# Performance work log

Hardware: AMD Instinct MI355X
Metric: run time of the kernel (lower is better)

Reference implementation:

```python
import jax, jax.numpy as jnp
import numpy as np

N, P, H, K = 8192, 32, 512, 100
D = 2 * P
R = 32  # min(32, max(8, H))


def setup_inputs() -> dict:
    key = jax.random.key(0)
    ks = jax.random.split(key, 12)
    # strictly increasing event times
    dts = jax.random.uniform(ks[0], (N,), dtype=jnp.float32) * 0.1 + 1e-3
    times = jnp.cumsum(dts)
    marks = jax.random.randint(ks[1], (N,), 0, K, dtype=jnp.int32)
    u_inputs = jax.random.normal(ks[2], (N, H), dtype=jnp.float32) * 0.1
    # parameters (match torch init scales)
    lambda_log_real = jax.random.normal(ks[3], (P,), dtype=jnp.float32) * 0.1
    lambda_im = jax.random.normal(ks[4], (P,), dtype=jnp.float32) * 0.05
    V = jnp.eye(D, dtype=jnp.float32) + 0.01 * jax.random.normal(ks[5], (D, D), dtype=jnp.float32)
    B = jax.random.normal(ks[6], (D, H), dtype=jnp.float32) * 0.05
    E = jax.random.normal(ks[7], (D, R), dtype=jnp.float32) * 0.05
    alpha = jax.random.normal(ks[8], (R, K), dtype=jnp.float32) * 0.05
    gate_w = jax.random.normal(ks[9], (P, H), dtype=jnp.float32) * 0.02
    gate_b = jax.random.normal(ks[10], (P,), dtype=jnp.float32) * 0.02
    x0 = jnp.zeros((D,), dtype=jnp.float32)
    return {"times": times, "marks": marks, "u_inputs": u_inputs,
            "lambda_log_real": lambda_log_real, "lambda_im": lambda_im,
            "V": V, "B": B, "E": E, "alpha": alpha,
            "gate_w": gate_w, "gate_b": gate_b, "x0": x0}


def _v_block(V, pr, pi):
    """V @ blockdiag_p([[pr,-pi],[pi,pr]]) for each step n. V:(D,D), pr/pi:(n,P) -> (n,D,D)."""
    Dd = V.shape[0]
    Pp = pr.shape[-1]
    Vr = V.reshape(Dd, Pp, 2)
    col0 = Vr[None, :, :, 0] * pr[:, None, :] + Vr[None, :, :, 1] * pi[:, None, :]
    col1 = -Vr[None, :, :, 0] * pi[:, None, :] + Vr[None, :, :, 1] * pr[:, None, :]
    return jnp.stack([col0, col1], axis=-1).reshape(-1, Dd, Dd)


def reference(times, marks, u_inputs, lambda_log_real, lambda_im, V, B, E, alpha, gate_w, gate_b, x0):
    n = times.shape[0]
    dt = jnp.concatenate([times[:1], jnp.diff(times)])  # (N,) t_0 - 0, t_i - t_{i-1}
    # input-dependent eigenvalues: real = -softplus(log_real) * softplus(Wu+b), imag fixed
    gate = jax.nn.softplus(u_inputs @ gate_w.T + gate_b)           # (N,P)
    real = -jax.nn.softplus(lambda_log_real)[None, :] * gate        # (N,P)
    imag = jnp.broadcast_to(lambda_im[None, :], real.shape)         # (N,P)
    dtc = dt[:, None]
    exps = jnp.exp(real * dtc)
    cosb = jnp.cos(imag * dtc)
    sinb = jnp.sin(imag * dtc)
    a = exps * cosb  # Re(exp(lam dt))
    c = exps * sinb  # Im(exp(lam dt))
    V_inv = jnp.linalg.inv(V)
    # exp(A dt) = V M V^{-1}, M block-rotation per mode
    Aexp = _v_block(V, a, c) @ V_inv                                # (N,D,D)
    # integral (exp(lam dt) - 1)/lam, with dt fallback near lam=0
    denom = real * real + imag * imag
    num_re = a - 1.0
    num_im = c
    qr = (num_re * real + num_im * imag) / (denom + 1e-12)
    qi = (num_im * real - num_re * imag) / (denom + 1e-12)
    small = denom < 1e-8
    qr = jnp.where(small, dtc, qr)
    qi = jnp.where(small, 0.0, qi)
    VMint = _v_block(V, qr, qi)                                     # (N,D,D)
    # cont = V M_int V^{-1} B u  (fuse V^{-1} B u first, avoiding Kmat materialization)
    w = u_inputs @ (V_inv @ B).T                                    # (N,D)
    cont = jnp.einsum('nij,nj->ni', VMint, w)
    cont = jnp.where(dtc > 0, cont, 0.0)
    # mark impulses r_k = E alpha[:, k]
    r = (E @ alpha)[:, marks].T                                     # (N,D)

    def step(x_prev, inp):
        A_i, c_i, r_i = inp
        x_left = A_i @ x_prev + c_i
        x_right = x_left + r_i
        return x_right, (x_right, x_left)

    _, (x_right, x_left) = jax.lax.scan(step, x0, (Aexp, cont, r))
    return x_right, x_left
```

## Files before the change

kernel.cpp:

```cpp
#include <hip/hip_runtime.h>
#include <math.h>

#define NN 8192
#define PP 32
#define HH 512
#define KK 100
#define DD 64
#define RR 32
#define MM 96

#define CH 2
#define CPB 16
#define SB 32
#define NB 256

#define OFF_VINV   0
#define OFF_M      (OFF_VINV + DD*DD)
#define OFF_EAT    (OFF_M + DD*HH)
#define OFF_RHT    (OFF_EAT + KK*DD)
#define OFF_Y0     (OFF_RHT + KK*DD)
#define OFF_BAGG   (OFF_Y0 + DD)
#define OFF_YB     (OFF_BAGG + NB*PP*4)
#define OFF_C      (OFF_YB + NB*PP*2)
#define OFF_COEF   (OFF_C + NN*MM)

__device__ __forceinline__ float sp_fast(float x) {
    return x > 15.f ? x : __logf(1.f + __expf(x));
}
__device__ __forceinline__ float rcp_fast(float x) {
    float r;
    asm("v_rcp_f32 %0, %1" : "=v"(r) : "v"(x));
    return r;
}
__device__ __forceinline__ float4 comp_aff(float4 f, float4 g) {
    float4 r;
    r.x = f.x * g.x - f.y * g.y;
    r.y = f.x * g.y + f.y * g.x;
    r.z = f.x * g.z - f.y * g.w + f.z;
    r.w = f.x * g.w + f.y * g.z + f.w;
    return r;
}

#define IDX(r,c) ((r)*64 + ((c) ^ (((r)&7)<<2)))
__global__ __launch_bounds__(512) void kinv(const float* __restrict__ V,
                                            const float* __restrict__ x0,
                                            float* __restrict__ ws) {
    __shared__ float sm[16384];
    float* Vt = sm;
    float* X  = sm + 4096;
    float* Xt = sm + 8192;
    float* T  = sm + 12288;
    const int t  = threadIdx.x;
    const int j0 = (t & 15) << 2;
    const int i0 = (t >> 4) << 1;

    float nx[2][4];
    #pragma unroll
    for (int r = 0; r < 2; r++) {
        float4 v4 = *(const float4*)&V[(i0 + r) * DD + j0];
        float vv[4] = {v4.x, v4.y, v4.z, v4.w};
        #pragma unroll
        for (int s = 0; s < 4; s++) {
            Vt[IDX(j0 + s, i0 + r)] = vv[s];
            float xv = ((i0 + r) == (j0 + s) ? 2.f : 0.f) - vv[s];
            nx[r][s] = xv;
            Xt[IDX(j0 + s, i0 + r)] = xv;
        }
        *(float4*)&X[IDX(i0 + r, j0)] = make_float4(nx[r][0], nx[r][1], nx[r][2], nx[r][3]);
    }
    __syncthreads();

    for (int it = 0; it < 3; it++) {
        float acc[2][4];
        #pragma unroll
        for (int r = 0; r < 2; r++)
            #pragma unroll
            for (int s = 0; s < 4; s++) acc[r][s] = 0.f;
        for (int k = 0; k < DD; k++) {
            float2 a2 = *(float2*)&Vt[IDX(k, i0)];
            float4 b4 = *(float4*)&X[IDX(k, j0)];
            float bv[4] = {b4.x, b4.y, b4.z, b4.w};
            #pragma unroll
            for (int s = 0; s < 4; s++) {
                acc[0][s] = fmaf(a2.x, bv[s], acc[0][s]);
                acc[1][s] = fmaf(a2.y, bv[s], acc[1][s]);
            }
        }
        #pragma unroll
        for (int r = 0; r < 2; r++)
            *(float4*)&T[IDX(i0 + r, j0)] = make_float4(acc[r][0], acc[r][1], acc[r][2], acc[r][3]);
        __syncthreads();
        #pragma unroll
        for (int r = 0; r < 2; r++)
            #pragma unroll
            for (int s = 0; s < 4; s++) acc[r][s] = 0.f;
        for (int k = 0; k < DD; k++) {
            float2 a2 = *(float2*)&Xt[IDX(k, i0)];
            float4 b4 = *(float4*)&T[IDX(k, j0)];
            float bv[4] = {b4.x, b4.y, b4.z, b4.w};
            #pragma unroll
            for (int s = 0; s < 4; s++) {
                acc[0][s] = fmaf(a2.x, bv[s], acc[0][s]);
                acc[1][s] = fmaf(a2.y, bv[s], acc[1][s]);
            }
        }
        #pragma unroll
        for (int r = 0; r < 2; r++) {
            float4 xo = *(float4*)&X[IDX(i0 + r, j0)];
            nx[r][0] = 2.f * xo.x - acc[r][0];
            nx[r][1] = 2.f * xo.y - acc[r][1];
            nx[r][2] = 2.f * xo.z - acc[r][2];
            nx[r][3] = 2.f * xo.w - acc[r][3];
        }
        __syncthreads();
        #pragma unroll
        for (int r = 0; r < 2; r++) {
            *(float4*)&X[IDX(i0 + r, j0)] = make_float4(nx[r][0], nx[r][1], nx[r][2], nx[r][3]);
            #pragma unroll
            for (int s = 0; s < 4; s++) Xt[IDX(j0 + s, i0 + r)] = nx[r][s];
        }
        __syncthreads();
    }
    #pragma unroll
    for (int r = 0; r < 2; r++)
        *(float4*)&ws[OFF_VINV + (i0 + r) * DD + j0] =
            make_float4(nx[r][0], nx[r][1], nx[r][2], nx[r][3]);
    float4 xq = *(const float4*)&x0[j0];
    float xw[4] = {xq.x, xq.y, xq.z, xq.w};
    #pragma unroll
    for (int r = 0; r < 2; r++) {
        float pr = nx[r][0] * xw[0] + nx[r][1] * xw[1] + nx[r][2] * xw[2] + nx[r][3] * xw[3];
        T[(i0 + r) * 17 + (t & 15)] = pr;
    }
    __syncthreads();
    if (t < DD) {
        float s = 0.f;
        #pragma unroll
        for (int jt = 0; jt < 16; jt++) s += T[t * 17 + jt];
        ws[OFF_Y0 + t] = s;
    }
}

__global__ __launch_bounds__(256) void kpre(const float* __restrict__ B,
                                            const float* __restrict__ E,
                                            const float* __restrict__ alpha,
                                            float* __restrict__ ws) {
    int b = blockIdx.x, t = threadIdx.x;
    if (b < 32) {
        int d = b * 2 + (t >> 7);
        int h0 = (t & 127) * 4;
        const float* vr = ws + OFF_VINV + d * DD;
        float4 acc = {0.f, 0.f, 0.f, 0.f};
        for (int j = 0; j < DD; j++) {
            float v = vr[j];
            float4 b4 = *(const float4*)&B[j * HH + h0];
            acc.x = fmaf(v, b4.x, acc.x); acc.y = fmaf(v, b4.y, acc.y);
            acc.z = fmaf(v, b4.z, acc.z); acc.w = fmaf(v, b4.w, acc.w);
        }
        *(float4*)&ws[OFF_M + d * HH + h0] = acc;
    } else {
        __shared__ float vi[DD * 65];
        __shared__ float ea_s[4][DD];
        int kk = (b - 32) * 4 + (t >> 6);
        int d = t & 63;
        for (int idx = t; idx < DD * DD; idx += 256)
            vi[(idx >> 6) * 65 + (idx & 63)] = ws[OFF_VINV + idx];
        float ea = 0.f;
        #pragma unroll
        for (int r = 0; r < RR; r++) ea = fmaf(E[d * RR + r], alpha[r * KK + kk], ea);
        ws[OFF_EAT + kk * DD + d] = ea;
        ea_s[t >> 6][d] = ea;
        __syncthreads();
        float rr = 0.f;
        for (int j = 0; j < DD; j++) rr = fmaf(vi[d * 65 + j], ea_s[t >> 6][j], rr);
        ws[OFF_RHT + kk * DD + d] = rr;
    }
}

__global__ __launch_bounds__(256, 2) void kgemm(const float* __restrict__ u,
                                                const float* __restrict__ gate_w,
                                                float* __restrict__ ws) {
    __shared__ float uT[16 * 64];
    __shared__ float mT[96 * 64];
    int t = threadIdx.x;
    int n0 = blockIdx.x * 16;
    int tn = t & 7, tm = t >> 3;
    float acc[2][3];
    #pragma unroll
    for (int i = 0; i < 2; i++)
        #pragma unroll
        for (int j = 0; j < 3; j++) acc[i][j] = 0.f;

    for (int kc = 0; kc < HH; kc += 64) {
        {
            int r = t >> 4, c4 = t & 15;
            float4 f4 = *(const float4*)&u[(n0 + r) * HH + kc + c4 * 4];
            *(float4*)&uT[r * 64 + ((c4 ^ (r & 7)) << 2)] = f4;
        }
        #pragma unroll
        for (int s = 0; s < 6; s++) {
            int idx = t + 256 * s;
            int r = idx >> 4, c4 = idx & 15;
            const float* src = (r < 32) ? &gate_w[r * HH] : &ws[OFF_M + (r - 32) * HH];
            float4 f4 = *(const float4*)&src[kc + c4 * 4];
            *(float4*)&mT[r * 64 + ((c4 ^ (r & 7)) << 2)] = f4;
        }
        __syncthreads();
        #pragma unroll
        for (int k4 = 0; k4 < 16; k4++) {
            float4 uu[2], mm[3];
            #pragma unroll
            for (int i = 0; i < 2; i++) {
                int rr = 2 * tn + i;
                uu[i] = *(float4*)&uT[rr * 64 + ((k4 ^ (rr & 7)) << 2)];
            }
            #pragma unroll
            for (int j = 0; j < 3; j++) {
                int m = 3 * tm + j;
                mm[j] = *(float4*)&mT[m * 64 + ((k4 ^ (m & 7)) << 2)];
            }
            #pragma unroll
            for (int i = 0; i < 2; i++)
                #pragma unroll
                for (int j = 0; j < 3; j++)
                    acc[i][j] += uu[i].x * mm[j].x + uu[i].y * mm[j].y +
                                 uu[i].z * mm[j].z + uu[i].w * mm[j].w;
        }
        __syncthreads();
    }
    #pragma unroll
    for (int i = 0; i < 2; i++)
        #pragma unroll
        for (int j = 0; j < 3; j++)
            ws[OFF_C + (n0 + 2 * tn + i) * MM + 3 * tm + j] = acc[i][j];
}

__device__ __forceinline__ float4 coef_fast(const float* __restrict__ ws,
                                            const int* __restrict__ marks,
                                            int n, int p, float dtv,
                                            float nlr, float imag, float gb) {
    float gate = sp_fast(ws[OFF_C + n * MM + p] + gb);
    float real = nlr * gate;
    float e = __expf(real * dtv);
    float x = imag * dtv, x2 = x * x;
    float cb = 1.f - x2 * (0.5f - x2 * (1.f / 24.f));
    float sb = x * (1.f - x2 * ((1.f / 6.f) - x2 * (1.f / 120.f)));
    float a = e * cb, c = e * sb;
    float denom = real * real + imag * imag;
    float inv = rcp_fast(denom + 1e-12f);
    float nre = a - 1.f, nim = c;
    float qr = (nre * real + nim * imag) * inv;
    float qi = (nim * real - nre * imag) * inv;
    if (denom < 1e-8f) { qr = dtv; qi = 0.f; }
    float2 w = *(const float2*)&ws[OFF_C + n * MM + 32 + 2 * p];
    float br = qr * w.x - qi * w.y;
    float bi = qr * w.y + qi * w.x;
    if (!(dtv > 0.f)) { br = 0.f; bi = 0.f; }
    int mk = marks[n];
    float2 rh = *(const float2*)&ws[OFF_RHT + mk * DD + 2 * p];
    return make_float4(a, c, br + rh.x, bi + rh.y);
}

__global__ __launch_bounds__(512, 2) void kagg(const float* __restrict__ times,
                                               const int* __restrict__ marks,
                                               const float* __restrict__ llr,
                                               const float* __restrict__ lim,
                                               const float* __restrict__ gate_b,
                                               float* __restrict__ ws) {
    __shared__ float4 smagg[CPB][PP];
    int b = blockIdx.x, t = threadIdx.x;
    int c = t >> 5, p = t & 31;
    int n0 = b * SB + c * CH;
    float nlr = -sp_fast(llr[p]);
    float imag = lim[p], gb = gate_b[p];
    float tprev = (n0 == 0) ? 0.f : times[n0 - 1];
    float4* coef = (float4*)(ws + OFF_COEF);
    float4 agg = make_float4(1.f, 0.f, 0.f, 0.f);
    #pragma unroll
    for (int i = 0; i < CH; i++) {
        int n = n0 + i;
        float tcur = times[n];
        float dtv = tcur - tprev; tprev = tcur;
        float4 cf = coef_fast(ws, marks, n, p, dtv, nlr, imag, gb);
        coef[n * PP + p] = cf;
        agg = comp_aff(cf, agg);
    }
    smagg[c][p] = agg;
    __syncthreads();
    if (t < PP) {
        float4 T = make_float4(1.f, 0.f, 0.f, 0.f);
        #pragma unroll
        for (int cc = 0; cc < CPB; cc++) T = comp_aff(smagg[cc][t], T);
        *(float4*)&ws[OFF_BAGG + (b * PP + t) * 4] = T;
    }
}

__global__ __launch_bounds__(256) void kscan(float* __restrict__ ws) {
    __shared__ float4 sseg[8][PP];
    __shared__ float4 qseg[8][PP];
    int t = threadIdx.x;
    int p = t & 31, s = t >> 5;
    const float4* bagg = (const float4*)(ws + OFF_BAGG);
    float4 S = make_float4(1.f, 0.f, 0.f, 0.f);
    for (int b = 32 * s; b < 32 * s + 32; b++) S = comp_aff(bagg[b * PP + p], S);
    sseg[s][p] = S;
    __syncthreads();
    if (t < PP) {
        float4 Q = make_float4(1.f, 0.f, 0.f, 0.f);
        #pragma unroll
        for (int ss = 0; ss < 8; ss++) { qseg[ss][t] = Q; Q = comp_aff(sseg[ss][t], Q); }
    }
    __syncthreads();
    float2 y0v = *(const float2*)&ws[OFF_Y0 + 2 * p];
    float4 Q = qseg[s][p];
    float2 y;
    y.x = Q.x * y0v.x - Q.y * y0v.y + Q.z;
    y.y = Q.x * y0v.y + Q.y * y0v.x + Q.w;
    for (int b = 32 * s; b < 32 * s + 32; b++) {
        *(float2*)&ws[OFF_YB + (b * PP + p) * 2] = y;
        float4 A = bagg[b * PP + p];
        float nyr = A.x * y.x - A.y * y.y + A.z;
        float nyi = A.x * y.y + A.y * y.x + A.w;
        y.x = nyr; y.y = nyi;
    }
}

__global__ __launch_bounds__(512, 2) void kout(const float* __restrict__ V,
                                               const int* __restrict__ marks,
                                               const float* __restrict__ ws,
                                               float* __restrict__ out) {
    __shared__ float vt[DD * 68];
    __shared__ float yl[SB * 68];
    __shared__ float4 smagg[CPB][PP];
    int b = blockIdx.x, t = threadIdx.x;
    #pragma unroll
    for (int s = 0; s < 8; s++) {
        int idx = t + 512 * s;
        vt[(idx & 63) * 68 + (idx >> 6)] = V[idx];
    }
    int c = t >> 5, p = t & 31;
    int n0 = b * SB + c * CH;
    const float4* coef = (const float4*)(ws + OFF_COEF);
    float4 cf0 = coef[(n0 + 0) * PP + p];
    float4 cf1 = coef[(n0 + 1) * PP + p];
    smagg[c][p] = comp_aff(cf1, cf0);
    __syncthreads();
    float2 y = *(const float2*)&ws[OFF_YB + (b * PP + p) * 2];
    #pragma unroll
    for (int cc = 0; cc < CPB - 1; cc++) {
        float4 A = smagg[cc][p];
        if (cc < c) {
            float nyr = A.x * y.x - A.y * y.y + A.z;
            float nyi = A.x * y.y + A.y * y.x + A.w;
            y.x = nyr; y.y = nyi;
        }
    }
    {
        float nyr = cf0.x * y.x - cf0.y * y.y + cf0.z;
        float nyi = cf0.x * y.y + cf0.y * y.x + cf0.w;
        y.x = nyr; y.y = nyi;
        *(float2*)&yl[(c * CH + 0) * 68 + 2 * p] = y;
        nyr = cf1.x * y.x - cf1.y * y.y + cf1.z;
        nyi = cf1.x * y.y + cf1.y * y.x + cf1.w;
        y.x = nyr; y.y = nyi;
        *(float2*)&yl[(c * CH + 1) * 68 + 2 * p] = y;
    }
    __syncthreads();
    int dt4 = (t & 15) * 4;
    int nr = t >> 4;
    float acc[4] = {0.f, 0.f, 0.f, 0.f};
    for (int k = 0; k < DD; k++) {
        float4 vv = *(float4*)&vt[k * 68 + dt4];
        float yv = yl[nr * 68 + k];
        acc[0] = fmaf(yv, vv.x, acc[0]);
        acc[1] = fmaf(yv, vv.y, acc[1]);
        acc[2] = fmaf(yv, vv.z, acc[2]);
        acc[3] = fmaf(yv, vv.w, acc[3]);
    }
    int n = b * SB + nr;
    int mk = marks[n];
    float4 o4 = make_float4(acc[0], acc[1], acc[2], acc[3]);
    *(float4*)&out[n * DD + dt4] = o4;
    float4 e4 = *(const float4*)&ws[OFF_EAT + mk * DD + dt4];
    o4.x -= e4.x; o4.y -= e4.y; o4.z -= e4.z; o4.w -= e4.w;
    *(float4*)&out[NN * DD + n * DD + dt4] = o4;
}

extern "C" void kernel_launch(void* const* d_in, const int* in_sizes, int n_in,
                              void* d_out, int out_size, void* d_ws, size_t ws_size,
                              hipStream_t stream) {
    (void)in_sizes; (void)n_in; (void)out_size; (void)ws_size;
    const float* times  = (const float*)d_in[0];
    const int*   marks  = (const int*)d_in[1];
    const float* u      = (const float*)d_in[2];
    const float* llr    = (const float*)d_in[3];
    const float* lim    = (const float*)d_in[4];
    const float* V      = (const float*)d_in[5];
    const float* B      = (const float*)d_in[6];
    const float* E      = (const float*)d_in[7];
    const float* alpha  = (const float*)d_in[8];
    const float* gate_w = (const float*)d_in[9];
    const float* gate_b = (const float*)d_in[10];
    const float* x0     = (const float*)d_in[11];
    float* ws  = (float*)d_ws;
    float* out = (float*)d_out;

    hipLaunchKernelGGL(kinv,  dim3(1),   dim3(512), 0, stream, V, x0, ws);
    hipLaunchKernelGGL(kpre,  dim3(57),  dim3(256), 0, stream, B, E, alpha, ws);
    hipLaunchKernelGGL(kgemm, dim3(512), dim3(256), 0, stream, u, gate_w, ws);
    hipLaunchKernelGGL(kagg,  dim3(256), dim3(512), 0, stream, times, marks, llr, lim, gate_b, ws);
    hipLaunchKernelGGL(kscan, dim3(1),   dim3(256), 0, stream, ws);
    hipLaunchKernelGGL(kout,  dim3(256), dim3(512), 0, stream, V, marks, ws, out);
}
```

Baseline: 166.6 us.

## Fuse six kernels into one cooperative megakernel with grid syncs

Replaces the six launches (inverse, precompute, gemm, aggregate, serial scan, output) with a single cooperative kernel of 256 blocks, separated into three phases by grid-wide syncs. The gemm now multiplies by B directly, and V^{-1} is applied afterwards per block, which removes the dependency on the inverse before the gemm. The single-block serial scan becomes a per-block prefix over the block aggregates. This is meant to remove launch overhead and serial stages, but block 0 does the Newton inverse while the other blocks proceed, and each block recomputes up to 256 prefix compositions. If the cooperative launch fails, it falls back to three ordinary launches.

```diff
diff --git a/kernel.cpp b/kernel.cpp
--- a/kernel.cpp
+++ b/kernel.cpp
@@ -1,5 +1,8 @@
 #include <hip/hip_runtime.h>
+#include <hip/hip_cooperative_groups.h>
 #include <math.h>
+
+namespace cg = cooperative_groups;
 
 #define NN 8192
 #define PP 32
@@ -8,21 +11,23 @@
 #define DD 64
 #define RR 32
 #define MM 96
-
-#define CH 2
-#define CPB 16
 #define SB 32
-#define NB 256
-
-#define OFF_VINV   0
-#define OFF_M      (OFF_VINV + DD*DD)
-#define OFF_EAT    (OFF_M + DD*HH)
-#define OFF_RHT    (OFF_EAT + KK*DD)
-#define OFF_Y0     (OFF_RHT + KK*DD)
-#define OFF_BAGG   (OFF_Y0 + DD)
-#define OFF_YB     (OFF_BAGG + NB*PP*4)
-#define OFF_C      (OFF_YB + NB*PP*2)
-#define OFF_COEF   (OFF_C + NN*MM)
+#define NSEG 256
+
+#define OFF_VINV 0
+#define OFF_EAT  4096
+#define OFF_RHT  10496
+#define OFF_Y0   16896
+#define OFF_BAGG 16960
+#define OFF_C    49728
+#define OFF_COEF 836160
+
+#define L1_CT   4352
+#define L1_AG   7424
+#define L2_AG   4352
+#define L2_PREF 6400
+#define L2_YL   8448
+#define L2_YB   10624
 
 __device__ __forceinline__ float sp_fast(float x) {
     return x > 15.f ? x : __logf(1.f + __expf(x));
@@ -42,348 +47,326 @@
 }
 
 #define IDX(r,c) ((r)*64 + ((c) ^ (((r)&7)<<2)))
-__global__ __launch_bounds__(512) void kinv(const float* __restrict__ V,
-                                            const float* __restrict__ x0,
-                                            float* __restrict__ ws) {
+
+__global__ void __launch_bounds__(512) mega(
+    const float* __restrict__ times, const int* __restrict__ marks,
+    const float* __restrict__ u, const float* __restrict__ llr,
+    const float* __restrict__ lim, const float* __restrict__ V,
+    const float* __restrict__ B, const float* __restrict__ E,
+    const float* __restrict__ alpha, const float* __restrict__ gate_w,
+    const float* __restrict__ gate_b, const float* __restrict__ x0,
+    float* __restrict__ ws, float* __restrict__ out, int phase) {
     __shared__ float sm[16384];
-    float* Vt = sm;
-    float* X  = sm + 4096;
-    float* Xt = sm + 8192;
-    float* T  = sm + 12288;
-    const int t  = threadIdx.x;
-    const int j0 = (t & 15) << 2;
-    const int i0 = (t >> 4) << 1;
-
-    float nx[2][4];
-    #pragma unroll
-    for (int r = 0; r < 2; r++) {
-        float4 v4 = *(const float4*)&V[(i0 + r) * DD + j0];
-        float vv[4] = {v4.x, v4.y, v4.z, v4.w};
+    cg::grid_group grid = cg::this_grid();
+    const int b = blockIdx.x, t = threadIdx.x;
+
+    if (phase & 1) {
+        if (b == 0) {
+            float* Vt = sm;
+            float* X  = sm + 4096;
+            float* Xt = sm + 8192;
+            float* T  = sm + 12288;
+            const int i0 = ((t & 255) >> 4) << 2;
+            const int j0 = (t & 15) << 2;
+            float nx[4][4];
+            if (t < 256) {
+                #pragma unroll
+                for (int r = 0; r < 4; r++) {
+                    float4 v4 = *(const float4*)&V[(i0 + r) * DD + j0];
+                    float vv[4] = {v4.x, v4.y, v4.z, v4.w};
+                    #pragma unroll
+                    for (int s = 0; s < 4; s++) {
+                        Vt[IDX(j0 + s, i0 + r)] = vv[s];
+                        float xv = ((i0 + r) == (j0 + s) ? 2.f : 0.f) - vv[s];
+                        nx[r][s] = xv;
+                        Xt[IDX(j0 + s, i0 + r)] = xv;
+                    }
+                    *(float4*)&X[IDX(i0 + r, j0)] =
+                        make_float4(nx[r][0], nx[r][1], nx[r][2], nx[r][3]);
+                }
+            }
+            __syncthreads();
+            for (int it = 0; it < 3; it++) {
+                float ac[4][4];
+                if (t < 256) {
+                    #pragma unroll
+                    for (int r = 0; r < 4; r++)
+                        #pragma unroll
+                        for (int s = 0; s < 4; s++) ac[r][s] = 0.f;
+                    for (int k = 0; k < DD; k++) {
+                        float4 a4 = *(float4*)&Vt[IDX(k, i0)];
+                        float4 b4 = *(float4*)&X[IDX(k, j0)];
+                        float av[4] = {a4.x, a4.y, a4.z, a4.w};
+                        float bv[4] = {b4.x, b4.y, b4.z, b4.w};
+                        #pragma unroll
+                        for (int r = 0; r < 4; r++)
+                            #pragma unroll
+                            for (int s = 0; s < 4; s++)
+                                ac[r][s] = fmaf(av[r], bv[s], ac[r][s]);
+                    }
+                    #pragma unroll
+                    for (int r = 0; r < 4; r++)
+                        *(float4*)&T[IDX(i0 + r, j0)] =
+                            make_float4(ac[r][0], ac[r][1], ac[r][2], ac[r][3]);
+                }
+                __syncthreads();
+                if (t < 256) {
+                    #pragma unroll
+                    for (int r = 0; r < 4; r++)
+                        #pragma unroll
+                        for (int s = 0; s < 4; s++) ac[r][s] = 0.f;
+                    for (int k = 0; k < DD; k++) {
+                        float4 a4 = *(float4*)&Xt[IDX(k, i0)];
+                        float4 b4 = *(float4*)&T[IDX(k, j0)];
+                        float av[4] = {a4.x, a4.y, a4.z, a4.w};
+                        float bv[4] = {b4.x, b4.y, b4.z, b4.w};
+                        #pragma unroll
+                        for (int r = 0; r < 4; r++)
+                            #pragma unroll
+                            for (int s = 0; s < 4; s++)
+                                ac[r][s] = fmaf(av[r], bv[s], ac[r][s]);
+                    }
+                    #pragma unroll
+                    for (int r = 0; r < 4; r++) {
+                        float4 xo = *(float4*)&X[IDX(i0 + r, j0)];
+                        nx[r][0] = 2.f * xo.x - ac[r][0];
+                        nx[r][1] = 2.f * xo.y - ac[r][1];
+                        nx[r][2] = 2.f * xo.z - ac[r][2];
+                        nx[r][3] = 2.f * xo.w - ac[r][3];
+                    }
+                }
+                __syncthreads();
+                if (t < 256) {
+                    #pragma unroll
+                    for (int r = 0; r < 4; r++) {
+                        *(float4*)&X[IDX(i0 + r, j0)] =
+                            make_float4(nx[r][0], nx[r][1], nx[r][2], nx[r][3]);
+                        #pragma unroll
+                        for (int s = 0; s < 4; s++) Xt[IDX(j0 + s, i0 + r)] = nx[r][s];
+                    }
+                }
+                __syncthreads();
+            }
+            if (t < 256) {
+                #pragma unroll
+                for (int r = 0; r < 4; r++)
+                    *(float4*)&ws[OFF_VINV + (i0 + r) * DD + j0] =
+                        make_float4(nx[r][0], nx[r][1], nx[r][2], nx[r][3]);
+            }
+            for (int idx = t; idx < KK * DD; idx += 512) {
+                int k = idx >> 6, d = idx & 63;
+                float ea = 0.f;
+                #pragma unroll
+                for (int r = 0; r < RR; r++)
+                    ea = fmaf(E[d * RR + r], alpha[r * KK + k], ea);
+                ws[OFF_EAT + idx] = ea;
+                if (k < 64) Vt[k * 64 + d] = ea; else T[(k - 64) * 64 + d] = ea;
+            }
+            __syncthreads();
+            for (int idx = t; idx < KK * DD; idx += 512) {
+                int k = idx >> 6, d = idx & 63;
+                const float* ea = (k < 64) ? &Vt[k * 64] : &T[(k - 64) * 64];
+                float rr = 0.f;
+                for (int j = 0; j < DD; j++) rr = fmaf(Xt[IDX(j, d)], ea[j], rr);
+                ws[OFF_RHT + idx] = rr;
+            }
+            if (t < DD) {
+                float s = 0.f;
+                for (int j = 0; j < DD; j++) s = fmaf(Xt[IDX(j, t)], x0[j], s);
+                ws[OFF_Y0 + t] = s;
+            }
+            __syncthreads();
+        }
+        {
+            float* uT = sm;
+            float* mT = sm + 2048;
+            const int n0 = b * SB;
+            const int tn = t & 15, tm = t >> 4;
+            float acc0 = 0.f, acc1 = 0.f, acc2 = 0.f,
+                  acc3 = 0.f, acc4 = 0.f, acc5 = 0.f;
+            for (int kc = 0; kc < HH; kc += 64) {
+                {
+                    int r = t >> 4, c4 = t & 15;
+                    float4 f4 = *(const float4*)&u[(n0 + r) * HH + kc + c4 * 4];
+                    *(float4*)&uT[r * 64 + ((c4 ^ (r & 7)) << 2)] = f4;
+                }
+                #pragma unroll
+                for (int s2 = 0; s2 < 3; s2++) {
+                    int idx = t + 512 * s2;
+                    int r = idx >> 4, c4 = idx & 15;
+                    const float* src = (r < 32) ? &gate_w[r * HH] : &B[(r - 32) * HH];
+                    float4 f4 = *(const float4*)&src[kc + c4 * 4];
+                    *(float4*)&mT[r * 64 + ((c4 ^ (r & 7)) << 2)] = f4;
+                }
+                __syncthreads();
+                #pragma unroll
+                for (int k4 = 0; k4 < 16; k4++) {
+                    float4 uu[2], mm[3];
+                    #pragma unroll
+                    for (int i = 0; i < 2; i++) {
+                        int rr = 2 * tn + i;
+                        uu[i] = *(float4*)&uT[rr * 64 + ((k4 ^ (rr & 7)) << 2)];
+                    }
+                    #pragma unroll
+                    for (int j = 0; j < 3; j++) {
+                        int m = 3 * tm + j;
+                        mm[j] = *(float4*)&mT[m * 64 + ((k4 ^ (m & 7)) << 2)];
+                    }
+                    acc0 += uu[0].x*mm[0].x + uu[0].y*mm[0].y + uu[0].z*mm[0].z + uu[0].w*mm[0].w;
+                    acc1 += uu[0].x*mm[1].x + uu[0].y*mm[1].y + uu[0].z*mm[1].z + uu[0].w*mm[1].w;
+                    acc2 += uu[0].x*mm[2].x + uu[0].y*mm[2].y + uu[0].z*mm[2].z + uu[0].w*mm[2].w;
+                    acc3 += uu[1].x*mm[0].x + uu[1].y*mm[0].y + uu[1].z*mm[0].z + uu[1].w*mm[0].w;
+                    acc4 += uu[1].x*mm[1].x + uu[1].y*mm[1].y + uu[1].z*mm[1].z + uu[1].w*mm[1].w;
+                    acc5 += uu[1].x*mm[2].x + uu[1].y*mm[2].y + uu[1].z*mm[2].z + uu[1].w*mm[2].w;
+                }
+                __syncthreads();
+            }
+            float* Cw = ws + OFF_C + (size_t)b * SB * MM;
+            Cw[(2*tn+0) * MM + 3*tm+0] = acc0;
+            Cw[(2*tn+0) * MM + 3*tm+1] = acc1;
+            Cw[(2*tn+0) * MM + 3*tm+2] = acc2;
+            Cw[(2*tn+1) * MM + 3*tm+0] = acc3;
+            Cw[(2*tn+1) * MM + 3*tm+1] = acc4;
+            Cw[(2*tn+1) * MM + 3*tm+2] = acc5;
+        }
+    }
+    if (phase == 7) { __threadfence(); grid.sync(); }
+
+    if (phase & 2) {
+        const int n0 = b * SB;
+        for (int idx = t; idx < DD * DD; idx += 512) {
+            int d = idx >> 6, j = idx & 63;
+            sm[j * 68 + d] = ws[OFF_VINV + idx];
+        }
+        for (int idx = t; idx < SB * MM; idx += 512)
+            sm[L1_CT + idx] = ws[OFF_C + (size_t)b * SB * MM + idx];
+        __syncthreads();
+        {
+            const int nl = t >> 4, d0 = (t & 15) << 2;
+            float4 a = {0.f, 0.f, 0.f, 0.f};
+            for (int j = 0; j < DD; j++) {
+                float cr = sm[L1_CT + nl * MM + 32 + j];
+                float4 v4 = *(float4*)&sm[j * 68 + d0];
+                a.x = fmaf(cr, v4.x, a.x); a.y = fmaf(cr, v4.y, a.y);
+                a.z = fmaf(cr, v4.z, a.z); a.w = fmaf(cr, v4.w, a.w);
+            }
+            __syncthreads();
+            *(float4*)&sm[L1_CT + nl * MM + 32 + d0] = a;
+        }
+        __syncthreads();
+        const int c = t >> 5, p = t & 31;
+        const float nlr = -sp_fast(llr[p]);
+        const float imag = lim[p], gb = gate_b[p];
+        float4 cfs[2];
         #pragma unroll
-        for (int s = 0; s < 4; s++) {
-            Vt[IDX(j0 + s, i0 + r)] = vv[s];
-            float xv = ((i0 + r) == (j0 + s) ? 2.f : 0.f) - vv[s];
-            nx[r][s] = xv;
-            Xt[IDX(j0 + s, i0 + r)] = xv;
-        }
-        *(float4*)&X[IDX(i0 + r, j0)] = make_float4(nx[r][0], nx[r][1], nx[r][2], nx[r][3]);
+        for (int i = 0; i < 2; i++) {
+            int nl = c * 2 + i, n = n0 + nl;
+            float dtv = times[n] - (n ? times[n - 1] : 0.f);
+            float gate = sp_fast(sm[L1_CT + nl * MM + p] + gb);
+            float real = nlr * gate;
+            float e = __expf(real * dtv);
+            float x = imag * dtv, x2 = x * x;
+            float cb = 1.f - x2 * (0.5f - x2 * (1.f / 24.f));
+            float sb = x * (1.f - x2 * ((1.f / 6.f) - x2 * (1.f / 120.f)));
+            float a = e * cb, cc = e * sb;
+            float denom = real * real + imag * imag;
+            float inv = rcp_fast(denom + 1e-12f);
+            float nre = a - 1.f, nim = cc;
+            float qr = (nre * real + nim * imag) * inv;
+            float qi = (nim * real - nre * imag) * inv;
+            if (denom < 1e-8f) { qr = dtv; qi = 0.f; }
+            float2 w = *(float2*)&sm[L1_CT + nl * MM + 32 + 2 * p];
+            float br = qr * w.x - qi * w.y;
+            float bi = qr * w.y + qi * w.x;
+            if (!(dtv > 0.f)) { br = 0.f; bi = 0.f; }
+            int mk = marks[n];
+            float2 rh = *(const float2*)&ws[OFF_RHT + mk * DD + 2 * p];
+            cfs[i] = make_float4(a, cc, br + rh.x, bi + rh.y);
+            *(float4*)&ws[OFF_COEF + ((size_t)n * PP + p) * 4] = cfs[i];
+        }
+        ((float4*)(sm + L1_AG))[c * 32 + p] = comp_aff(cfs[1], cfs[0]);
+        __syncthreads();
+        if (t < PP) {
+            float4 T = make_float4(1.f, 0.f, 0.f, 0.f);
+            #pragma unroll
+            for (int cc = 0; cc < 16; cc++)
+                T = comp_aff(((float4*)(sm + L1_AG))[cc * 32 + t], T);
+            *(float4*)&ws[OFF_BAGG + (b * PP + t) * 4] = T;
+        }
     }
-    __syncthreads();
-
-    for (int it = 0; it < 3; it++) {
-        float acc[2][4];
-        #pragma unroll
-        for (int r = 0; r < 2; r++)
+    if (phase == 7) { __threadfence(); grid.sync(); }
+
+    if (phase & 4) {
+        const int n0 = b * SB;
+        const int c = t >> 5, p = t & 31;
+        for (int idx = t; idx < DD * DD; idx += 512) {
+            int d = idx >> 6, k = idx & 63;
+            sm[k * 68 + d] = V[idx];
+        }
+        float4 cf0 = *(float4*)&ws[OFF_COEF + ((size_t)(n0 + c * 2)     * PP + p) * 4];
+        float4 cf1 = *(float4*)&ws[OFF_COEF + ((size_t)(n0 + c * 2 + 1) * PP + p) * 4];
+        float4* ag   = (float4*)(sm + L2_AG);
+        float4* pref = (float4*)(sm + L2_PREF);
+        float2* yb   = (float2*)(sm + L2_YB);
+        ag[c * 32 + p] = comp_aff(cf1, cf0);
+        {
+            int q0 = c * 16, q1 = min(b, q0 + 16);
+            float4 Q = make_float4(1.f, 0.f, 0.f, 0.f);
+            for (int q = q0; q < q1; q++)
+                Q = comp_aff(*(const float4*)&ws[OFF_BAGG + (q * PP + p) * 4], Q);
+            pref[c * 32 + p] = Q;
+        }
+        __syncthreads();
+        if (t < PP) {
+            float2 y = *(const float2*)&ws[OFF_Y0 + 2 * t];
             #pragma unroll
-            for (int s = 0; s < 4; s++) acc[r][s] = 0.f;
-        for (int k = 0; k < DD; k++) {
-            float2 a2 = *(float2*)&Vt[IDX(k, i0)];
-            float4 b4 = *(float4*)&X[IDX(k, j0)];
-            float bv[4] = {b4.x, b4.y, b4.z, b4.w};
+            for (int jg = 0; jg < 16; jg++) {
+                float4 Q = pref[jg * 32 + t];
+                float nyr = Q.x * y.x - Q.y * y.y + Q.z;
+                float nyi = Q.x * y.y + Q.y * y.x + Q.w;
+                y.x = nyr; y.y = nyi;
+            }
+            yb[t] = y;
+        }
+        __syncthreads();
+        {
+            float2 y = yb[p];
             #pragma unroll
-            for (int s = 0; s < 4; s++) {
-                acc[0][s] = fmaf(a2.x, bv[s], acc[0][s]);
-                acc[1][s] = fmaf(a2.y, bv[s], acc[1][s]);
-            }
-        }
-        #pragma unroll
-        for (int r = 0; r < 2; r++)
-            *(float4*)&T[IDX(i0 + r, j0)] = make_float4(acc[r][0], acc[r][1], acc[r][2], acc[r][3]);
-        __syncthreads();
-        #pragma unroll
-        for (int r = 0; r < 2; r++)
-            #pragma unroll
-            for (int s = 0; s < 4; s++) acc[r][s] = 0.f;
-        for (int k = 0; k < DD; k++) {
-            float2 a2 = *(float2*)&Xt[IDX(k, i0)];
-            float4 b4 = *(float4*)&T[IDX(k, j0)];
-            float bv[4] = {b4.x, b4.y, b4.z, b4.w};
-            #pragma unroll
-            for (int s = 0; s < 4; s++) {
-                acc[0][s] = fmaf(a2.x, bv[s], acc[0][s]);
-                acc[1][s] = fmaf(a2.y, bv[s], acc[1][s]);
-            }
-        }
-        #pragma unroll
-        for (int r = 0; r < 2; r++) {
-            float4 xo = *(float4*)&X[IDX(i0 + r, j0)];
-            nx[r][0] = 2.f * xo.x - acc[r][0];
-            nx[r][1] = 2.f * xo.y - acc[r][1];
-            nx[r][2] = 2.f * xo.z - acc[r][2];
-            nx[r][3] = 2.f * xo.w - acc[r][3];
-        }
-        __syncthreads();
-        #pragma unroll
-        for (int r = 0; r < 2; r++) {
-            *(float4*)&X[IDX(i0 + r, j0)] = make_float4(nx[r][0], nx[r][1], nx[r][2], nx[r][3]);
-            #pragma unroll
-            for (int s = 0; s < 4; s++) Xt[IDX(j0 + s, i0 + r)] = nx[r][s];
-        }
-        __syncthreads();
+            for (int cc = 0; cc < 15; cc++) {
+                if (cc < c) {
+                    float4 A = ag[cc * 32 + p];
+                    float nyr = A.x * y.x - A.y * y.y + A.z;
+                    float nyi = A.x * y.y + A.y * y.x + A.w;
+                    y.x = nyr; y.y = nyi;
+                }
+            }
+            float nyr = cf0.x * y.x - cf0.y * y.y + cf0.z;
+            float nyi = cf0.x * y.y + cf0.y * y.x + cf0.w;
+            y.x = nyr; y.y = nyi;
+            *(float2*)&sm[L2_YL + (c * 2 + 0) * 68 + 2 * p] = y;
+            nyr = cf1.x * y.x - cf1.y * y.y + cf1.z;
+            nyi = cf1.x * y.y + cf1.y * y.x + cf1.w;
+            y.x = nyr; y.y = nyi;
+            *(float2*)&sm[L2_YL + (c * 2 + 1) * 68 + 2 * p] = y;
+        }
+        __syncthreads();
+        {
+            const int nr = t >> 4, d0 = (t & 15) << 2;
+            float4 a = {0.f, 0.f, 0.f, 0.f};
+            for (int k = 0; k < DD; k++) {
+                float yv = sm[L2_YL + nr * 68 + k];
+                float4 v4 = *(float4*)&sm[k * 68 + d0];
+                a.x = fmaf(yv, v4.x, a.x); a.y = fmaf(yv, v4.y, a.y);
+                a.z = fmaf(yv, v4.z, a.z); a.w = fmaf(yv, v4.w, a.w);
+            }
+            int n = n0 + nr;
+            int mk = marks[n];
+            *(float4*)&out[(size_t)n * DD + d0] = a;
+            float4 e4 = *(const float4*)&ws[OFF_EAT + mk * DD + d0];
+            a.x -= e4.x; a.y -= e4.y; a.z -= e4.z; a.w -= e4.w;
+            *(float4*)&out[(size_t)NN * DD + (size_t)n * DD + d0] = a;
+        }
     }
-    #pragma unroll
-    for (int r = 0; r < 2; r++)
-        *(float4*)&ws[OFF_VINV + (i0 + r) * DD + j0] =
-            make_float4(nx[r][0], nx[r][1], nx[r][2], nx[r][3]);
-    float4 xq = *(const float4*)&x0[j0];
-    float xw[4] = {xq.x, xq.y, xq.z, xq.w};
-    #pragma unroll
-    for (int r = 0; r < 2; r++) {
-        float pr = nx[r][0] * xw[0] + nx[r][1] * xw[1] + nx[r][2] * xw[2] + nx[r][3] * xw[3];
-        T[(i0 + r) * 17 + (t & 15)] = pr;
-    }
-    __syncthreads();
-    if (t < DD) {
-        float s = 0.f;
-        #pragma unroll
-        for (int jt = 0; jt < 16; jt++) s += T[t * 17 + jt];
-        ws[OFF_Y0 + t] = s;
-    }
-}
-
-__global__ __launch_bounds__(256) void kpre(const float* __restrict__ B,
-                                            const float* __restrict__ E,
-                                            const float* __restrict__ alpha,
-                                            float* __restrict__ ws) {
-    int b = blockIdx.x, t = threadIdx.x;
-    if (b < 32) {
-        int d = b * 2 + (t >> 7);
-        int h0 = (t & 127) * 4;
-        const float* vr = ws + OFF_VINV + d * DD;
-        float4 acc = {0.f, 0.f, 0.f, 0.f};
-        for (int j = 0; j < DD; j++) {
-            float v = vr[j];
-            float4 b4 = *(const float4*)&B[j * HH + h0];
-            acc.x = fmaf(v, b4.x, acc.x); acc.y = fmaf(v, b4.y, acc.y);
-            acc.z = fmaf(v, b4.z, acc.z); acc.w = fmaf(v, b4.w, acc.w);
-        }
-        *(float4*)&ws[OFF_M + d * HH + h0] = acc;
-    } else {
-        __shared__ float vi[DD * 65];
-        __shared__ float ea_s[4][DD];
-        int kk = (b - 32) * 4 + (t >> 6);
-        int d = t & 63;
-        for (int idx = t; idx < DD * DD; idx += 256)
-            vi[(idx >> 6) * 65 + (idx & 63)] = ws[OFF_VINV + idx];
-        float ea = 0.f;
-        #pragma unroll
-        for (int r = 0; r < RR; r++) ea = fmaf(E[d * RR + r], alpha[r * KK + kk], ea);
-        ws[OFF_EAT + kk * DD + d] = ea;
-        ea_s[t >> 6][d] = ea;
-        __syncthreads();
-        float rr = 0.f;
-        for (int j = 0; j < DD; j++) rr = fmaf(vi[d * 65 + j], ea_s[t >> 6][j], rr);
-        ws[OFF_RHT + kk * DD + d] = rr;
-    }
-}
-
-__global__ __launch_bounds__(256, 2) void kgemm(const float* __restrict__ u,
-                                                const float* __restrict__ gate_w,
-                                                float* __restrict__ ws) {
-    __shared__ float uT[16 * 64];
-    __shared__ float mT[96 * 64];
-    int t = threadIdx.x;
-    int n0 = blockIdx.x * 16;
-    int tn = t & 7, tm = t >> 3;
-    float acc[2][3];
-    #pragma unroll
-    for (int i = 0; i < 2; i++)
-        #pragma unroll
-        for (int j = 0; j < 3; j++) acc[i][j] = 0.f;
-
-    for (int kc = 0; kc < HH; kc += 64) {
-        {
-            int r = t >> 4, c4 = t & 15;
-            float4 f4 = *(const float4*)&u[(n0 + r) * HH + kc + c4 * 4];
-            *(float4*)&uT[r * 64 + ((c4 ^ (r & 7)) << 2)] = f4;
-        }
-        #pragma unroll
-        for (int s = 0; s < 6; s++) {
-            int idx = t + 256 * s;
-            int r = idx >> 4, c4 = idx & 15;
-            const float* src = (r < 32) ? &gate_w[r * HH] : &ws[OFF_M + (r - 32) * HH];
-            float4 f4 = *(const float4*)&src[kc + c4 * 4];
-            *(float4*)&mT[r * 64 + ((c4 ^ (r & 7)) << 2)] = f4;
-        }
-        __syncthreads();
-        #pragma unroll
-        for (int k4 = 0; k4 < 16; k4++) {
-            float4 uu[2], mm[3];
-            #pragma unroll
-            for (int i = 0; i < 2; i++) {
-                int rr = 2 * tn + i;
-                uu[i] = *(float4*)&uT[rr * 64 + ((k4 ^ (rr & 7)) << 2)];
-            }
-            #pragma unroll
-            for (int j = 0; j < 3; j++) {
-                int m = 3 * tm + j;
-                mm[j] = *(float4*)&mT[m * 64 + ((k4 ^ (m & 7)) << 2)];
-            }
-            #pragma unroll
-            for (int i = 0; i < 2; i++)
-                #pragma unroll
-                for (int j = 0; j < 3; j++)
-                    acc[i][j] += uu[i].x * mm[j].x + uu[i].y * mm[j].y +
-                                 uu[i].z * mm[j].z + uu[i].w * mm[j].w;
-        }
-        __syncthreads();
-    }
-    #pragma unroll
-    for (int i = 0; i < 2; i++)
-        #pragma unroll
-        for (int j = 0; j < 3; j++)
-            ws[OFF_C + (n0 + 2 * tn + i) * MM + 3 * tm + j] = acc[i][j];
-}
-
-__device__ __forceinline__ float4 coef_fast(const float* __restrict__ ws,
-                                            const int* __restrict__ marks,
-                                            int n, int p, float dtv,
-                                            float nlr, float imag, float gb) {
-    float gate = sp_fast(ws[OFF_C + n * MM + p] + gb);
-    float real = nlr * gate;
-    float e = __expf(real * dtv);
-    float x = imag * dtv, x2 = x * x;
-    float cb = 1.f - x2 * (0.5f - x2 * (1.f / 24.f));
-    float sb = x * (1.f - x2 * ((1.f / 6.f) - x2 * (1.f / 120.f)));
-    float a = e * cb, c = e * sb;
-    float denom = real * real + imag * imag;
-    float inv = rcp_fast(denom + 1e-12f);
-    float nre = a - 1.f, nim = c;
-    float qr = (nre * real + nim * imag) * inv;
-    float qi = (nim * real - nre * imag) * inv;
-    if (denom < 1e-8f) { qr = dtv; qi = 0.f; }
-    float2 w = *(const float2*)&ws[OFF_C + n * MM + 32 + 2 * p];
-    float br = qr * w.x - qi * w.y;
-    float bi = qr * w.y + qi * w.x;
-    if (!(dtv > 0.f)) { br = 0.f; bi = 0.f; }
-    int mk = marks[n];
-    float2 rh = *(const float2*)&ws[OFF_RHT + mk * DD + 2 * p];
-    return make_float4(a, c, br + rh.x, bi + rh.y);
-}
-
-__global__ __launch_bounds__(512, 2) void kagg(const float* __restrict__ times,
-                                               const int* __restrict__ marks,
-                                               const float* __restrict__ llr,
-                                               const float* __restrict__ lim,
-                                               const float* __restrict__ gate_b,
-                                               float* __restrict__ ws) {
-    __shared__ float4 smagg[CPB][PP];
-    int b = blockIdx.x, t = threadIdx.x;
-    int c = t >> 5, p = t & 31;
-    int n0 = b * SB + c * CH;
-    float nlr = -sp_fast(llr[p]);
-    float imag = lim[p], gb = gate_b[p];
-    float tprev = (n0 == 0) ? 0.f : times[n0 - 1];
-    float4* coef = (float4*)(ws + OFF_COEF);
-    float4 agg = make_float4(1.f, 0.f, 0.f, 0.f);
-    #pragma unroll
-    for (int i = 0; i < CH; i++) {
-        int n = n0 + i;
-        float tcur = times[n];
-        float dtv = tcur - tprev; tprev = tcur;
-        float4 cf = coef_fast(ws, marks, n, p, dtv, nlr, imag, gb);
-        coef[n * PP + p] = cf;
-        agg = comp_aff(cf, agg);
-    }
-    smagg[c][p] = agg;
-    __syncthreads();
-    if (t < PP) {
-        float4 T = make_float4(1.f, 0.f, 0.f, 0.f);
-        #pragma unroll
-        for (int cc = 0; cc < CPB; cc++) T = comp_aff(smagg[cc][t], T);
-        *(float4*)&ws[OFF_BAGG + (b * PP + t) * 4] = T;
-    }
-}
-
-__global__ __launch_bounds__(256) void kscan(float* __restrict__ ws) {
-    __shared__ float4 sseg[8][PP];
-    __shared__ float4 qseg[8][PP];
-    int t = threadIdx.x;
-    int p = t & 31, s = t >> 5;
-    const float4* bagg = (const float4*)(ws + OFF_BAGG);
-    float4 S = make_float4(1.f, 0.f, 0.f, 0.f);
-    for (int b = 32 * s; b < 32 * s + 32; b++) S = comp_aff(bagg[b * PP + p], S);
-    sseg[s][p] = S;
-    __syncthreads();
-    if (t < PP) {
-        float4 Q = make_float4(1.f, 0.f, 0.f, 0.f);
-        #pragma unroll
-        for (int ss = 0; ss < 8; ss++) { qseg[ss][t] = Q; Q = comp_aff(sseg[ss][t], Q); }
-    }
-    __syncthreads();
-    float2 y0v = *(const float2*)&ws[OFF_Y0 + 2 * p];
-    float4 Q = qseg[s][p];
-    float2 y;
-    y.x = Q.x * y0v.x - Q.y * y0v.y + Q.z;
-    y.y = Q.x * y0v.y + Q.y * y0v.x + Q.w;
-    for (int b = 32 * s; b < 32 * s + 32; b++) {
-        *(float2*)&ws[OFF_YB + (b * PP + p) * 2] = y;
-        float4 A = bagg[b * PP + p];
-        float nyr = A.x * y.x - A.y * y.y + A.z;
-        float nyi = A.x * y.y + A.y * y.x + A.w;
-        y.x = nyr; y.y = nyi;
-    }
-}
-
-__global__ __launch_bounds__(512, 2) void kout(const float* __restrict__ V,
-                                               const int* __restrict__ marks,
-                                               const float* __restrict__ ws,
-                                               float* __restrict__ out) {
-    __shared__ float vt[DD * 68];
-    __shared__ float yl[SB * 68];
-    __shared__ float4 smagg[CPB][PP];
-    int b = blockIdx.x, t = threadIdx.x;
-    #pragma unroll
-    for (int s = 0; s < 8; s++) {
-        int idx = t + 512 * s;
-        vt[(idx & 63) * 68 + (idx >> 6)] = V[idx];
-    }
-    int c = t >> 5, p = t & 31;
-    int n0 = b * SB + c * CH;
-    const float4* coef = (const float4*)(ws + OFF_COEF);
-    float4 cf0 = coef[(n0 + 0) * PP + p];
-    float4 cf1 = coef[(n0 + 1) * PP + p];
-    smagg[c][p] = comp_aff(cf1, cf0);
-    __syncthreads();
-    float2 y = *(const float2*)&ws[OFF_YB + (b * PP + p) * 2];
-    #pragma unroll
-    for (int cc = 0; cc < CPB - 1; cc++) {
-        float4 A = smagg[cc][p];
-        if (cc < c) {
-            float nyr = A.x * y.x - A.y * y.y + A.z;
-            float nyi = A.x * y.y + A.y * y.x + A.w;
-            y.x = nyr; y.y = nyi;
-        }
-    }
-    {
-        float nyr = cf0.x * y.x - cf0.y * y.y + cf0.z;
-        float nyi = cf0.x * y.y + cf0.y * y.x + cf0.w;
-        y.x = nyr; y.y = nyi;
-        *(float2*)&yl[(c * CH + 0) * 68 + 2 * p] = y;
-        nyr = cf1.x * y.x - cf1.y * y.y + cf1.z;
-        nyi = cf1.x * y.y + cf1.y * y.x + cf1.w;
-        y.x = nyr; y.y = nyi;
-        *(float2*)&yl[(c * CH + 1) * 68 + 2 * p] = y;
-    }
-    __syncthreads();
-    int dt4 = (t & 15) * 4;
-    int nr = t >> 4;
-    float acc[4] = {0.f, 0.f, 0.f, 0.f};
-    for (int k = 0; k < DD; k++) {
-        float4 vv = *(float4*)&vt[k * 68 + dt4];
-        float yv = yl[nr * 68 + k];
-        acc[0] = fmaf(yv, vv.x, acc[0]);
-        acc[1] = fmaf(yv, vv.y, acc[1]);
-        acc[2] = fmaf(yv, vv.z, acc[2]);
-        acc[3] = fmaf(yv, vv.w, acc[3]);
-    }
-    int n = b * SB + nr;
-    int mk = marks[n];
-    float4 o4 = make_float4(acc[0], acc[1], acc[2], acc[3]);
-    *(float4*)&out[n * DD + dt4] = o4;
-    float4 e4 = *(const float4*)&ws[OFF_EAT + mk * DD + dt4];
-    o4.x -= e4.x; o4.y -= e4.y; o4.z -= e4.z; o4.w -= e4.w;
-    *(float4*)&out[NN * DD + n * DD + dt4] = o4;
 }
 
 extern "C" void kernel_launch(void* const* d_in, const int* in_sizes, int n_in,
@@ -405,10 +388,23 @@
     float* ws  = (float*)d_ws;
     float* out = (float*)d_out;
 
-    hipLaunchKernelGGL(kinv,  dim3(1),   dim3(512), 0, stream, V, x0, ws);
-    hipLaunchKernelGGL(kpre,  dim3(57),  dim3(256), 0, stream, B, E, alpha, ws);
-    hipLaunchKernelGGL(kgemm, dim3(512), dim3(256), 0, stream, u, gate_w, ws);
-    hipLaunchKernelGGL(kagg,  dim3(256), dim3(512), 0, stream, times, marks, llr, lim, gate_b, ws);
-    hipLaunchKernelGGL(kscan, dim3(1),   dim3(256), 0, stream, ws);
-    hipLaunchKernelGGL(kout,  dim3(256), dim3(512), 0, stream, V, marks, ws, out);
+    int phase = 7;
+    void* args[] = { (void*)&times, (void*)&marks, (void*)&u, (void*)&llr,
+                     (void*)&lim, (void*)&V, (void*)&B, (void*)&E,
+                     (void*)&alpha, (void*)&gate_w, (void*)&gate_b, (void*)&x0,
+                     (void*)&ws, (void*)&out, (void*)&phase };
+    hipError_t err = hipLaunchCooperativeKernel(
+        reinterpret_cast<void*>(mega), dim3(NSEG), dim3(512), args, 0, stream);
+    if (err != hipSuccess) {
+        (void)hipGetLastError();
+        hipLaunchKernelGGL(mega, dim3(NSEG), dim3(512), 0, stream,
+                           times, marks, u, llr, lim, V, B, E, alpha,
+                           gate_w, gate_b, x0, ws, out, 1);
+        hipLaunchKernelGGL(mega, dim3(NSEG), dim3(512), 0, stream,
+                           times, marks, u, llr, lim, V, B, E, alpha,
+                           gate_w, gate_b, x0, ws, out, 2);
+        hipLaunchKernelGGL(mega, dim3(NSEG), dim3(512), 0, stream,
+                           times, marks, u, llr, lim, V, B, E, alpha,
+                           gate_w, gate_b, x0, ws, out, 4);
+    }
 }
```

Measured after the change: 327.8 us. 96.8% more time.
